# Kernel optimization log

Hardware: AMD Instinct MI355X
Metric: run time of the kernel (lower is better)

## Reference

```python
import jax, jax.numpy as jnp
import numpy as np

INPT, HID, NNODE, K, B = 64, 128, 10000, 16, 8

def setup_inputs() -> dict:
    key = jax.random.key(0)
    ks = jax.random.split(key, 12)
    def lin(k, fan_in, fan_out):
        # orthogonal-ish init stand-in; exact init values are irrelevant for the reference math
        return jax.random.normal(k, (fan_in, fan_out), jnp.float32) / np.sqrt(fan_in)
    return {
        "state": jax.random.normal(ks[0], (B, NNODE, INPT), jnp.float32),
        "internal": jax.random.normal(ks[1], (B, NNODE, INPT), jnp.float32),
        "state_neigh": jax.random.randint(ks[2], (NNODE, K), 0, NNODE),
        "internal_neigh": jax.random.randint(ks[3], (NNODE, K), 0, NNODE),
        "W1": lin(ks[4], INPT, HID), "b1": jnp.zeros((HID,), jnp.float32),
        "W2": lin(ks[5], HID, HID), "b2": jnp.zeros((HID,), jnp.float32),
        "Wu1": lin(ks[6], 2 * HID, HID), "bu1": jnp.zeros((HID,), jnp.float32),
        "Wu2": lin(ks[7], 2 * HID, HID), "bu2": jnp.zeros((HID,), jnp.float32),
    }

def _aggregate(se, ie, s_idx, i_idx):
    # se, ie: [B, N, H]; idx: [N, K] -> gather neighbors and sum over K
    g_s = jnp.take(se, s_idx, axis=1).sum(axis=2)   # [B, N, H]
    g_i = jnp.take(ie, i_idx, axis=1).sum(axis=2)   # [B, N, H]
    return g_s + g_i

def _update(aggr, h, W, b):
    x = jnp.concatenate((aggr, h), axis=-1)          # [B, N, 2H]
    return jax.nn.relu(x @ W + b)

def reference(state, internal, state_neigh, internal_neigh,
              W1, b1, W2, b2, Wu1, bu1, Wu2, bu2):
    # layer-1 embeddings
    state_embed = jax.nn.relu(state @ W1 + b1)       # [B, N, H]
    internal_embed = jax.nn.relu(internal @ W1 + b1)
    aggr1 = _aggregate(state_embed, internal_embed, state_neigh, internal_neigh)
    hu1 = _update(aggr1, internal_embed, Wu1, bu1)   # [B, N, H]
    # layer-2 embeddings
    se2 = jax.nn.relu(state_embed @ W2 + b2)
    ie2 = jax.nn.relu(hu1 @ W2 + b2)
    aggr2 = _aggregate(se2, ie2, state_neigh, internal_neigh)
    hu2 = _update(aggr2, ie2, Wu2, bu2)              # [B, N, H]
    return hu1, hu2
```

## Files before the change

kernel.cpp:

```cpp
#include <hip/hip_runtime.h>

#define HID 128
#define NNODE 10000
#define KN 16
#define ROWS 80000
#define NCHUNK 157
#define NTILES 2500

typedef __attribute__((ext_vector_type(8))) short short8;
typedef __attribute__((ext_vector_type(4))) float f32x4;
typedef __attribute__((ext_vector_type(2))) float f32x2;
typedef __attribute__((ext_vector_type(4))) unsigned int u32x4;
typedef __attribute__((ext_vector_type(2))) unsigned int u32x2;

__device__ __forceinline__ unsigned short f2b(float f) {
    unsigned u = __float_as_uint(f);
    u += 0x7FFFu + ((u >> 16) & 1u);
    return (unsigned short)(u >> 16);
}

__global__ __launch_bounds__(256) void wconv_all(
    const float* __restrict__ W1, const float* __restrict__ W2,
    const float* __restrict__ Wu1, const float* __restrict__ Wu2,
    unsigned short* __restrict__ W1t, unsigned short* __restrict__ W2t,
    unsigned short* __restrict__ Wu1t, unsigned short* __restrict__ Wu2t) {
    int idx = blockIdx.x * 256 + threadIdx.x;
    const float* W; unsigned short* Wt; int K; int off;
    if (idx < 8192)       { W = W1;  Wt = W1t;  K = 64;  off = idx; }
    else if (idx < 24576) { W = W2;  Wt = W2t;  K = 128; off = idx - 8192; }
    else if (idx < 57344) { W = Wu1; Wt = Wu1t; K = 256; off = idx - 24576; }
    else                  { W = Wu2; Wt = Wu2t; K = 256; off = idx - 57344; }
    int n = off & 127, k = off >> 7;
    Wt[n * K + k] = f2b(W[off]);
}

template<int K, bool AF32>
__global__ __launch_bounds__(512) void embed2(
    const void* __restrict__ A0, const void* __restrict__ A1,
    const unsigned short* __restrict__ Wt, const float* __restrict__ bias,
    unsigned short* __restrict__ Y0, unsigned short* __restrict__ Y1, int tot) {
    const int t = threadIdx.x, w = t >> 6, lane = t & 63;
    const int lrow = lane & 15, lk = lane >> 4;
    const int rs = w & 1, ng = w >> 1;
    const int col0 = ng * 32;

    short8 wf[2][K / 32];
    f32x4 bv[2];
#pragma unroll
    for (int p = 0; p < 2; ++p) {
        bv[p] = *(const f32x4*)(bias + col0 + p * 16 + lk * 4);
#pragma unroll
        for (int kt = 0; kt < K / 32; ++kt)
            wf[p][kt] = *(const short8*)(Wt + (col0 + p * 16 + lrow) * K + kt * 32 + lk * 8);
    }

    int T = blockIdx.x;
    if (T >= tot) return;

    auto loadx = [&](int TT, short8* xf) {
        const int half = TT >= NTILES;
        const void* A = half ? A1 : A0;
        const int row = (TT - half * NTILES) * 32 + rs * 16 + lrow;
        if constexpr (AF32) {
            const float* X = (const float*)A + (size_t)row * K;
#pragma unroll
            for (int kt = 0; kt < K / 32; ++kt) {
                f32x4 f0 = *(const f32x4*)(X + kt * 32 + lk * 8);
                f32x4 f1 = *(const f32x4*)(X + kt * 32 + lk * 8 + 4);
                short8 v;
#pragma unroll
                for (int e = 0; e < 4; ++e) { v[e] = (short)f2b(f0[e]); v[4 + e] = (short)f2b(f1[e]); }
                xf[kt] = v;
            }
        } else {
            const unsigned short* X = (const unsigned short*)A + (size_t)row * K;
#pragma unroll
            for (int kt = 0; kt < K / 32; ++kt)
                xf[kt] = *(const short8*)(X + kt * 32 + lk * 8);
        }
    };

    short8 xf[K / 32], xn[K / 32];
    loadx(T, xf);
    for (;;) {
        const int Tn = T + gridDim.x;
        const bool more = Tn < tot;
        if (more) loadx(Tn, xn);

        const int half = T >= NTILES;
        unsigned short* Y = half ? Y1 : Y0;
        const int row = (T - half * NTILES) * 32 + rs * 16 + lrow;
#pragma unroll
        for (int p = 0; p < 2; ++p) {
            f32x4 acc = {0.f, 0.f, 0.f, 0.f};
#pragma unroll
            for (int kt = 0; kt < K / 32; ++kt)
                acc = __builtin_amdgcn_mfma_f32_16x16x32_bf16(wf[p][kt], xf[kt], acc, 0, 0, 0);
            float v0 = acc[0] + bv[p][0]; v0 = v0 > 0.f ? v0 : 0.f;
            float v1 = acc[1] + bv[p][1]; v1 = v1 > 0.f ? v1 : 0.f;
            float v2 = acc[2] + bv[p][2]; v2 = v2 > 0.f ? v2 : 0.f;
            float v3 = acc[3] + bv[p][3]; v3 = v3 > 0.f ? v3 : 0.f;
            u32x2 ov = {(unsigned)f2b(v0) | ((unsigned)f2b(v1) << 16),
                        (unsigned)f2b(v2) | ((unsigned)f2b(v3) << 16)};
            *(u32x2*)(Y + (size_t)row * HID + col0 + p * 16 + lk * 4) = ov;
        }
        if (!more) break;
#pragma unroll
        for (int kt = 0; kt < K / 32; ++kt) xf[kt] = xn[kt];
        T = Tn;
    }
}

__global__ __launch_bounds__(512) void aggr_kernel(
    const unsigned short* __restrict__ SE, const unsigned short* __restrict__ IE,
    const int* __restrict__ sidx, const int* __restrict__ iidx,
    unsigned short* __restrict__ G) {
    __shared__ int sh_idx[64][33];
    const int t = threadIdx.x;
    const int b = blockIdx.x & 7;
    const int hc = blockIdx.x >> 3;
    const int h = hc >= NCHUNK ? 1 : 0;
    const int c = hc - h * NCHUNK;
    const int n0 = c * 64;

#pragma unroll
    for (int q = 0; q < 4; ++q) {
        const int e = t + q * 512;
        const int r = e >> 5, k = e & 31;
        int nr = n0 + r; if (nr > NNODE - 1) nr = NNODE - 1;
        sh_idx[r][k] = (k < KN) ? sidx[nr * KN + k] : iidx[nr * KN + (k - KN)];
    }
    __syncthreads();

    const int r = t >> 3, p = t & 7;
    const int col0 = h * 64 + p * 8;
    const int n = n0 + r;
    const size_t base = (size_t)b * NNODE * HID + col0;

    f32x2 acc[4];
#pragma unroll
    for (int w = 0; w < 4; ++w) acc[w] = (f32x2){0.f, 0.f};

#pragma unroll
    for (int q = 0; q < 4; ++q) {
        const unsigned short* P = (q < 2) ? SE : IE;
        u32x4 vals[8];
#pragma unroll
        for (int j = 0; j < 8; ++j)
            vals[j] = *(const u32x4*)(P + base + (size_t)sh_idx[r][q * 8 + j] * HID);
#pragma unroll
        for (int j = 0; j < 8; ++j)
#pragma unroll
            for (int w = 0; w < 4; ++w) {
                const unsigned u = vals[j][w];
                acc[w] += (f32x2){__uint_as_float(u << 16), __uint_as_float(u & 0xffff0000u)};
            }
    }

    if (n < NNODE) {
        short8 ov;
#pragma unroll
        for (int w = 0; w < 4; ++w) {
            ov[2 * w]     = (short)f2b(acc[w].x);
            ov[2 * w + 1] = (short)f2b(acc[w].y);
        }
        *(short8*)(G + ((size_t)b * NNODE + n) * HID + col0) = ov;
    }
}

__global__ __launch_bounds__(512) void update_gemm2(
    const unsigned short* __restrict__ G, const unsigned short* __restrict__ H,
    const unsigned short* __restrict__ Wut, const float* __restrict__ bu,
    float* __restrict__ Yf, unsigned short* __restrict__ Yb, int writeb) {
    const int t = threadIdx.x, w = t >> 6, lane = t & 63;
    const int lrow = lane & 15, lk = lane >> 4;
    const int rs = w & 1, ng = w >> 1;
    const int col0 = ng * 32;

    short8 wf[2][8];
    f32x4 bv[2];
#pragma unroll
    for (int p = 0; p < 2; ++p) {
        bv[p] = *(const f32x4*)(bu + col0 + p * 16 + lk * 4);
#pragma unroll
        for (int kt = 0; kt < 8; ++kt)
            wf[p][kt] = *(const short8*)(Wut + (col0 + p * 16 + lrow) * 256 + kt * 32 + lk * 8);
    }

    for (int T = blockIdx.x; T < NTILES; T += gridDim.x) {
        const int row = T * 32 + rs * 16 + lrow;
        short8 xf[8];
#pragma unroll
        for (int kt = 0; kt < 4; ++kt) {
            xf[kt]     = *(const short8*)(G + (size_t)row * HID + kt * 32 + lk * 8);
            xf[4 + kt] = *(const short8*)(H + (size_t)row * HID + kt * 32 + lk * 8);
        }
#pragma unroll
        for (int p = 0; p < 2; ++p) {
            f32x4 acc = {0.f, 0.f, 0.f, 0.f};
#pragma unroll
            for (int kt = 0; kt < 8; ++kt)
                acc = __builtin_amdgcn_mfma_f32_16x16x32_bf16(wf[p][kt], xf[kt], acc, 0, 0, 0);
            f32x4 o;
#pragma unroll
            for (int j = 0; j < 4; ++j) {
                float v = acc[j] + bv[p][j];
                o[j] = v > 0.f ? v : 0.f;
            }
            *(f32x4*)(Yf + (size_t)row * HID + col0 + p * 16 + lk * 4) = o;
            if (writeb) {
                u32x2 ov = {(unsigned)f2b(o[0]) | ((unsigned)f2b(o[1]) << 16),
                            (unsigned)f2b(o[2]) | ((unsigned)f2b(o[3]) << 16)};
                *(u32x2*)(Yb + (size_t)row * HID + col0 + p * 16 + lk * 4) = ov;
            }
        }
    }
}

extern "C" void kernel_launch(void* const* d_in, const int* in_sizes, int n_in,
                              void* d_out, int out_size, void* d_ws, size_t ws_size,
                              hipStream_t stream) {
    const float* state    = (const float*)d_in[0];
    const float* internal = (const float*)d_in[1];
    const int*   sidx     = (const int*)d_in[2];
    const int*   iidx     = (const int*)d_in[3];
    const float* W1  = (const float*)d_in[4];
    const float* b1  = (const float*)d_in[5];
    const float* W2  = (const float*)d_in[6];
    const float* b2  = (const float*)d_in[7];
    const float* Wu1 = (const float*)d_in[8];
    const float* bu1 = (const float*)d_in[9];
    const float* Wu2 = (const float*)d_in[10];
    const float* bu2 = (const float*)d_in[11];

    float* hu1 = (float*)d_out;
    float* hu2 = hu1 + (size_t)ROWS * HID;

    unsigned short* W1t  = (unsigned short*)d_ws;
    unsigned short* W2t  = W1t  + 64 * 128;
    unsigned short* Wu1t = W2t  + 128 * 128;
    unsigned short* Wu2t = Wu1t + 256 * 128;
    unsigned short* bufA = Wu2t + 256 * 128;
    unsigned short* bufB = bufA + (size_t)ROWS * HID;
    unsigned short* bufC = bufB + (size_t)ROWS * HID;
    unsigned short* bufD = bufC + (size_t)ROWS * HID;

    const size_t need4 = (size_t)90112 * 2 + 4 * (size_t)ROWS * HID * 2;
    const bool big = ws_size >= need4;

    dim3 b256(256), b512(512);
    const int AGRID = 8 * 2 * NCHUNK;

    wconv_all<<<352, b256, 0, stream>>>(W1, W2, Wu1, Wu2, W1t, W2t, Wu1t, Wu2t);

    embed2<64, true><<<1250, b512, 0, stream>>>(state, internal, W1t, b1, bufA, bufB, 2 * NTILES);

    if (big) {
        aggr_kernel<<<AGRID, b512, 0, stream>>>(bufA, bufB, sidx, iidx, bufD);
        update_gemm2<<<1250, b512, 0, stream>>>(bufD, bufB, Wu1t, bu1, hu1, bufC, 1);
        embed2<128, false><<<1250, b512, 0, stream>>>(bufA, bufC, W2t, b2, bufB, bufD, 2 * NTILES);
        aggr_kernel<<<AGRID, b512, 0, stream>>>(bufB, bufD, sidx, iidx, bufA);
        update_gemm2<<<1250, b512, 0, stream>>>(bufA, bufD, Wu2t, bu2, hu2, nullptr, 0);
    } else {
        unsigned short* Ghu2 = (unsigned short*)hu2;
        aggr_kernel<<<AGRID, b512, 0, stream>>>(bufA, bufB, sidx, iidx, Ghu2);
        update_gemm2<<<1250, b512, 0, stream>>>(Ghu2, bufB, Wu1t, bu1, hu1, bufC, 1);
        embed2<128, false><<<1250, b512, 0, stream>>>(bufA, nullptr, W2t, b2, bufB, nullptr, NTILES);
        embed2<128, false><<<1250, b512, 0, stream>>>(bufC, nullptr, W2t, b2, bufA, nullptr, NTILES);
        aggr_kernel<<<AGRID, b512, 0, stream>>>(bufB, bufA, sidx, iidx, bufC);
        update_gemm2<<<1250, b512, 0, stream>>>(bufC, bufA, Wu2t, bu2, hu2, nullptr, 0);
    }
}
```

Before: 231.9 us.

## Fuse neighbor aggregation with update GEMM via shared-memory tile

Merges the gather-sum aggregation kernel and the update GEMM into one kernel. Each block aggregates a 32-node tile across all 128 columns into a swizzled LDS buffer, then runs the MFMA update directly on it. This drops the global write and read of the intermediate aggregate buffer and one launch per layer. In exchange, each block must reload the update weights into registers, and the separate column-half split of the aggregation goes away, which changes parallelism per block.

```diff
diff --git a/kernel.cpp b/kernel.cpp
--- a/kernel.cpp
+++ b/kernel.cpp
@@ -4,8 +4,9 @@
 #define NNODE 10000
 #define KN 16
 #define ROWS 80000
-#define NCHUNK 157
 #define NTILES 2500
+#define ACHUNK 313
+#define AUGRID (8 * ACHUNK)
 
 typedef __attribute__((ext_vector_type(8))) short short8;
 typedef __attribute__((ext_vector_type(4))) float f32x4;
@@ -111,71 +112,68 @@
     }
 }
 
-__global__ __launch_bounds__(512) void aggr_kernel(
+__global__ __launch_bounds__(512) void k_aggr_update(
     const unsigned short* __restrict__ SE, const unsigned short* __restrict__ IE,
     const int* __restrict__ sidx, const int* __restrict__ iidx,
-    unsigned short* __restrict__ G) {
-    __shared__ int sh_idx[64][33];
+    const unsigned short* __restrict__ Wut, const float* __restrict__ bu,
+    float* __restrict__ Yf, unsigned short* __restrict__ Yb, int writeb) {
+    __shared__ int sh[32][33];
+    __shared__ __align__(16) unsigned short At[32 * 128];
     const int t = threadIdx.x;
     const int b = blockIdx.x & 7;
-    const int hc = blockIdx.x >> 3;
-    const int h = hc >= NCHUNK ? 1 : 0;
-    const int c = hc - h * NCHUNK;
-    const int n0 = c * 64;
-
-#pragma unroll
-    for (int q = 0; q < 4; ++q) {
+    const int n0 = (blockIdx.x >> 3) * 32;
+    const size_t gbase = (size_t)b * NNODE * HID;
+
+#pragma unroll
+    for (int q = 0; q < 2; ++q) {
         const int e = t + q * 512;
         const int r = e >> 5, k = e & 31;
         int nr = n0 + r; if (nr > NNODE - 1) nr = NNODE - 1;
-        sh_idx[r][k] = (k < KN) ? sidx[nr * KN + k] : iidx[nr * KN + (k - KN)];
+        sh[r][k] = (k < KN) ? sidx[nr * KN + k] : iidx[nr * KN + (k - KN)];
     }
     __syncthreads();
 
-    const int r = t >> 3, p = t & 7;
-    const int col0 = h * 64 + p * 8;
-    const int n = n0 + r;
-    const size_t base = (size_t)b * NNODE * HID + col0;
-
-    f32x2 acc[4];
-#pragma unroll
-    for (int w = 0; w < 4; ++w) acc[w] = (f32x2){0.f, 0.f};
-
-#pragma unroll
-    for (int q = 0; q < 4; ++q) {
-        const unsigned short* P = (q < 2) ? SE : IE;
-        u32x4 vals[8];
-#pragma unroll
-        for (int j = 0; j < 8; ++j)
-            vals[j] = *(const u32x4*)(P + base + (size_t)sh_idx[r][q * 8 + j] * HID);
-#pragma unroll
-        for (int j = 0; j < 8; ++j)
-#pragma unroll
-            for (int w = 0; w < 4; ++w) {
-                const unsigned u = vals[j][w];
-                acc[w] += (f32x2){__uint_as_float(u << 16), __uint_as_float(u & 0xffff0000u)};
-            }
-    }
-
-    if (n < NNODE) {
+    {
+        const int r = t >> 4, p = t & 15;
+        const int col0 = p * 8;
+        const size_t base = gbase + col0;
+
+        f32x2 acc[4];
+#pragma unroll
+        for (int w = 0; w < 4; ++w) acc[w] = (f32x2){0.f, 0.f};
+
+#pragma unroll
+        for (int q = 0; q < 4; ++q) {
+            const unsigned short* P = (q < 2) ? SE : IE;
+            u32x4 vals[8];
+#pragma unroll
+            for (int j = 0; j < 8; ++j)
+                vals[j] = *(const u32x4*)(P + base + (size_t)sh[r][q * 8 + j] * HID);
+#pragma unroll
+            for (int j = 0; j < 8; ++j)
+#pragma unroll
+                for (int w = 0; w < 4; ++w) {
+                    const unsigned u = vals[j][w];
+                    acc[w] += (f32x2){__uint_as_float(u << 16),
+                                      __uint_as_float(u & 0xffff0000u)};
+                }
+        }
         short8 ov;
 #pragma unroll
         for (int w = 0; w < 4; ++w) {
             ov[2 * w]     = (short)f2b(acc[w].x);
             ov[2 * w + 1] = (short)f2b(acc[w].y);
         }
-        *(short8*)(G + ((size_t)b * NNODE + n) * HID + col0) = ov;
-    }
-}
-
-__global__ __launch_bounds__(512) void update_gemm2(
-    const unsigned short* __restrict__ G, const unsigned short* __restrict__ H,
-    const unsigned short* __restrict__ Wut, const float* __restrict__ bu,
-    float* __restrict__ Yf, unsigned short* __restrict__ Yb, int writeb) {
-    const int t = threadIdx.x, w = t >> 6, lane = t & 63;
+        *(short8*)((char*)At + r * 256 + ((col0 * 2) ^ ((r & 7) << 4))) = ov;
+    }
+    __syncthreads();
+
+    const int w = t >> 6, lane = t & 63;
     const int lrow = lane & 15, lk = lane >> 4;
     const int rs = w & 1, ng = w >> 1;
     const int col0 = ng * 32;
+    const int rowl = rs * 16 + lrow;
+    const int n = n0 + rowl;
 
     short8 wf[2][8];
     f32x4 bv[2];
@@ -187,31 +185,39 @@
             wf[p][kt] = *(const short8*)(Wut + (col0 + p * 16 + lrow) * 256 + kt * 32 + lk * 8);
     }
 
-    for (int T = blockIdx.x; T < NTILES; T += gridDim.x) {
-        const int row = T * 32 + rs * 16 + lrow;
-        short8 xf[8];
-#pragma unroll
-        for (int kt = 0; kt < 4; ++kt) {
-            xf[kt]     = *(const short8*)(G + (size_t)row * HID + kt * 32 + lk * 8);
-            xf[4 + kt] = *(const short8*)(H + (size_t)row * HID + kt * 32 + lk * 8);
-        }
-#pragma unroll
-        for (int p = 0; p < 2; ++p) {
-            f32x4 acc = {0.f, 0.f, 0.f, 0.f};
-#pragma unroll
-            for (int kt = 0; kt < 8; ++kt)
-                acc = __builtin_amdgcn_mfma_f32_16x16x32_bf16(wf[p][kt], xf[kt], acc, 0, 0, 0);
-            f32x4 o;
-#pragma unroll
-            for (int j = 0; j < 4; ++j) {
-                float v = acc[j] + bv[p][j];
-                o[j] = v > 0.f ? v : 0.f;
-            }
-            *(f32x4*)(Yf + (size_t)row * HID + col0 + p * 16 + lk * 4) = o;
+    short8 xf[8];
+#pragma unroll
+    for (int kt = 0; kt < 4; ++kt)
+        xf[kt] = *(const short8*)((const char*)At + rowl * 256 +
+                                  ((kt * 64 + lk * 16) ^ ((rowl & 7) << 4)));
+    {
+        const int nh = n < NNODE ? n : NNODE - 1;
+        const unsigned short* Hrow = IE + gbase + (size_t)nh * HID;
+#pragma unroll
+        for (int kt = 0; kt < 4; ++kt)
+            xf[4 + kt] = *(const short8*)(Hrow + kt * 32 + lk * 8);
+    }
+
+    const bool ok = n < NNODE;
+    const size_t orow = gbase + (size_t)n * HID;
+#pragma unroll
+    for (int p = 0; p < 2; ++p) {
+        f32x4 acc = {0.f, 0.f, 0.f, 0.f};
+#pragma unroll
+        for (int kt = 0; kt < 8; ++kt)
+            acc = __builtin_amdgcn_mfma_f32_16x16x32_bf16(wf[p][kt], xf[kt], acc, 0, 0, 0);
+        f32x4 o;
+#pragma unroll
+        for (int j = 0; j < 4; ++j) {
+            float v = acc[j] + bv[p][j];
+            o[j] = v > 0.f ? v : 0.f;
+        }
+        if (ok) {
+            *(f32x4*)(Yf + orow + col0 + p * 16 + lk * 4) = o;
             if (writeb) {
                 u32x2 ov = {(unsigned)f2b(o[0]) | ((unsigned)f2b(o[1]) << 16),
                             (unsigned)f2b(o[2]) | ((unsigned)f2b(o[3]) << 16)};
-                *(u32x2*)(Yb + (size_t)row * HID + col0 + p * 16 + lk * 4) = ov;
+                *(u32x2*)(Yb + orow + col0 + p * 16 + lk * 4) = ov;
             }
         }
     }
@@ -237,37 +243,38 @@
     float* hu2 = hu1 + (size_t)ROWS * HID;
 
     unsigned short* W1t  = (unsigned short*)d_ws;
-    unsigned short* W2t  = W1t  + 64 * 128;
-    unsigned short* Wu1t = W2t  + 128 * 128;
-    unsigned short* Wu2t = Wu1t + 256 * 128;
-    unsigned short* bufA = Wu2t + 256 * 128;
-    unsigned short* bufB = bufA + (size_t)ROWS * HID;
-    unsigned short* bufC = bufB + (size_t)ROWS * HID;
-    unsigned short* bufD = bufC + (size_t)ROWS * HID;
-
-    const size_t need4 = (size_t)90112 * 2 + 4 * (size_t)ROWS * HID * 2;
-    const bool big = ws_size >= need4;
+    unsigned short* W2t  = W1t + 8192;
+    unsigned short* Wu1t = W2t + 16384;
+    unsigned short* Wu2t = Wu1t + 32768;
+    unsigned short* buf0 = Wu2t + 32768;
+    unsigned short* buf1 = buf0 + (size_t)ROWS * HID;
+    unsigned short* buf2 = buf1 + (size_t)ROWS * HID;
+    unsigned short* buf3 = buf2 + (size_t)ROWS * HID;
+
+    const size_t need_big = ((size_t)90112 + 4 * (size_t)ROWS * HID) * 2;
+    const bool big = ws_size >= need_big;
 
     dim3 b256(256), b512(512);
-    const int AGRID = 8 * 2 * NCHUNK;
 
     wconv_all<<<352, b256, 0, stream>>>(W1, W2, Wu1, Wu2, W1t, W2t, Wu1t, Wu2t);
 
-    embed2<64, true><<<1250, b512, 0, stream>>>(state, internal, W1t, b1, bufA, bufB, 2 * NTILES);
+    embed2<64, true><<<1250, b512, 0, stream>>>(state, internal, W1t, b1,
+                                                buf0, buf1, 2 * NTILES);
+
+    k_aggr_update<<<AUGRID, b512, 0, stream>>>(buf0, buf1, sidx, iidx,
+                                               Wu1t, bu1, hu1, buf2, 1);
 
     if (big) {
-        aggr_kernel<<<AGRID, b512, 0, stream>>>(bufA, bufB, sidx, iidx, bufD);
-        update_gemm2<<<1250, b512, 0, stream>>>(bufD, bufB, Wu1t, bu1, hu1, bufC, 1);
-        embed2<128, false><<<1250, b512, 0, stream>>>(bufA, bufC, W2t, b2, bufB, bufD, 2 * NTILES);
-        aggr_kernel<<<AGRID, b512, 0, stream>>>(bufB, bufD, sidx, iidx, bufA);
-        update_gemm2<<<1250, b512, 0, stream>>>(bufA, bufD, Wu2t, bu2, hu2, nullptr, 0);
+        embed2<128, false><<<1250, b512, 0, stream>>>(buf0, buf2, W2t, b2,
+                                                      buf3, buf1, 2 * NTILES);
+        k_aggr_update<<<AUGRID, b512, 0, stream>>>(buf3, buf1, sidx, iidx,
+                                                   Wu2t, bu2, hu2, nullptr, 0);
     } else {
-        unsigned short* Ghu2 = (unsigned short*)hu2;
-        aggr_kernel<<<AGRID, b512, 0, stream>>>(bufA, bufB, sidx, iidx, Ghu2);
-        update_gemm2<<<1250, b512, 0, stream>>>(Ghu2, bufB, Wu1t, bu1, hu1, bufC, 1);
-        embed2<128, false><<<1250, b512, 0, stream>>>(bufA, nullptr, W2t, b2, bufB, nullptr, NTILES);
-        embed2<128, false><<<1250, b512, 0, stream>>>(bufC, nullptr, W2t, b2, bufA, nullptr, NTILES);
-        aggr_kernel<<<AGRID, b512, 0, stream>>>(bufB, bufA, sidx, iidx, bufC);
-        update_gemm2<<<1250, b512, 0, stream>>>(bufC, bufA, Wu2t, bu2, hu2, nullptr, 0);
-    }
-}
+        embed2<128, false><<<1250, b512, 0, stream>>>(buf0, nullptr, W2t, b2,
+                                                      buf1, nullptr, NTILES);
+        embed2<128, false><<<1250, b512, 0, stream>>>(buf2, nullptr, W2t, b2,
+                                                      buf0, nullptr, NTILES);
+        k_aggr_update<<<AUGRID, b512, 0, stream>>>(buf1, buf0, sidx, iidx,
+                                                   Wu2t, bu2, hu2, nullptr, 0);
+    }
+}
```

After: 240.7 us. 3.8% more time.
